# Optimization experiments

Measured on AMD Instinct MI355X. Metric: run time of the kernel, lower is better.

The kernel has to match this reference:

```python
import jax, jax.numpy as jnp
import numpy as np

B, TQ, M, D, H, F, L = 4, 512, 512, 1024, 16, 4096, 6
S = D // H
R = TQ + M  # relative-attention length = memory + query
CUTOFFS = [20000, 40000, 200000]
PROJ_FACTOR = 4
LN_EPS = 1e-6
NEG_INF = -1e9


def setup_inputs() -> dict:
    key = jax.random.key(0)
    ks = iter(jax.random.split(key, 64))

    def w(shape, scale=0.02):
        return jax.random.normal(next(ks), shape, jnp.float32) * scale

    inp = {}
    inp['token_ids'] = jax.random.randint(next(ks), (B, TQ), 0, CUTOFFS[-1])
    inp['memories'] = w((L, B, M, D))
    starts = [0] + CUTOFFS
    pf = 1
    for i in range(len(CUTOFFS)):
        psize = max(1, D // pf)
        inp['emb_table%d' % i] = w((starts[i + 1] - starts[i], psize))
        inp['emb_proj%d' % i] = w((psize, D))
        pf *= PROJ_FACTOR
    inp['wq'] = w((L, D, H, S)); inp['wk'] = w((L, D, H, S))
    inp['wv'] = w((L, D, H, S)); inp['wr'] = w((L, D, H, S))
    inp['wo'] = w((L, H, S, D))
    inp['content_bias'] = w((L, H, S)); inp['position_bias'] = w((L, H, S))
    inp['ln1_scale'] = jnp.ones((L, D)); inp['ln1_bias'] = jnp.zeros((L, D))
    inp['ln2_scale'] = jnp.ones((L, D)); inp['ln2_bias'] = jnp.zeros((L, D))
    inp['ffn_w1'] = w((L, D, F)); inp['ffn_b1'] = jnp.zeros((L, F))
    inp['ffn_w2'] = w((L, F, D)); inp['ffn_b2'] = jnp.zeros((L, D))
    return inp


def layernorm(x, scale, bias):
    mu = jnp.mean(x, axis=-1, keepdims=True)
    var = jnp.var(x, axis=-1, keepdims=True)
    return (x - mu) * jax.lax.rsqrt(var + LN_EPS) * scale + bias


def rel_shift(x):
    # x: [B, H, Q, R] -> shifted so position j aligns with relative distance
    b, h, q, r = x.shape
    x = jnp.pad(x, ((0, 0), (0, 0), (0, 0), (1, 0)))
    x = x.reshape(b, h, r + 1, q)[:, :, 1:, :]
    return x.reshape(b, h, q, r)


def positional_encoding(r_len, d):
    pos = jnp.arange(r_len - 1, -1, -1, dtype=jnp.float32)  # r_len-1 ... 0
    inv_freq = 1.0 / (10000.0 ** (jnp.arange(0, d, 2, dtype=jnp.float32) / d))
    sinusoid = pos[:, None] * inv_freq[None, :]
    return jnp.concatenate([jnp.sin(sinusoid), jnp.cos(sinusoid)], axis=-1)


def adaptive_embed(ids, tables, projs):
    # jit-friendly version of AdaptiveEmbedding.compute_embeddings:
    # gather per-cluster, project up to D, combine via masks.
    d = projs[0].shape[-1]
    y = jnp.zeros(ids.shape + (d,), jnp.float32)
    starts = [0] + CUTOFFS
    for tab, proj, lo, hi in zip(tables, projs, starts[:-1], starts[1:]):
        mask = (ids >= lo) & (ids < hi)
        idx = jnp.clip(ids - lo, 0, tab.shape[0] - 1)
        emb = jnp.einsum('btp,pd->btd', tab[idx], proj)
        y = y + jnp.where(mask[..., None], emb, 0.0)
    return y * (d ** 0.5)


def transformer_xl(token_ids, memories, emb_tables, emb_projs, wq, wk, wv, wr,
                   wo, content_bias, position_bias, ln1_scale, ln1_bias,
                   ln2_scale, ln2_bias, ffn_w1, ffn_b1, ffn_w2, ffn_b2):
    x = adaptive_embed(token_ids, emb_tables, emb_projs)  # [B, TQ, D]
    pe = positional_encoding(R, D)                        # [R, D]
    q_idx = jnp.arange(TQ)[:, None]
    r_idx = jnp.arange(R)[None, :]
    future = r_idx > q_idx + M                            # [TQ, R], True=masked
    scale = 1.0 / np.sqrt(S).astype(np.float32)
    for l in range(L):
        q = jnp.einsum('btd,dhs->bths', x, wq[l])
        kv_in = jnp.concatenate([memories[l], x], axis=1)  # [B, R, D]
        k = jnp.einsum('brd,dhs->brhs', kv_in, wk[l])
        v = jnp.einsum('brd,dhs->brhs', kv_in, wv[l])
        r = jnp.einsum('rd,dhs->rhs', pe, wr[l])
        ac = jnp.einsum('bqhs,brhs->bhqr', q + content_bias[l], k)
        bd = rel_shift(jnp.einsum('bqhs,rhs->bhqr', q + position_bias[l], r))
        scores = (ac + bd) * scale
        scores = jnp.where(future[None, None], NEG_INF, scores)
        attn = jax.nn.softmax(scores, axis=-1)
        ctx = jnp.einsum('bhqr,brhs->bqhs', attn, v)
        out = jnp.einsum('bqhs,hsd->bqd', ctx, wo[l])
        x = layernorm(x + out, ln1_scale[l], ln1_bias[l])
        h = jax.nn.relu(jnp.einsum('btd,df->btf', x, ffn_w1[l]) + ffn_b1[l])
        h = jnp.einsum('btf,fd->btd', h, ffn_w2[l]) + ffn_b2[l]
        x = layernorm(x + h, ln2_scale[l], ln2_bias[l])
    return x


def reference(token_ids, memories, emb_table0, emb_proj0, emb_table1,
              emb_proj1, emb_table2, emb_proj2, wq, wk, wv, wr, wo,
              content_bias, position_bias, ln1_scale, ln1_bias, ln2_scale,
              ln2_bias, ffn_w1, ffn_b1, ffn_w2, ffn_b2):
    return transformer_xl(
        token_ids, memories,
        [emb_table0, emb_table1, emb_table2],
        [emb_proj0, emb_proj1, emb_proj2],
        wq, wk, wv, wr, wo, content_bias, position_bias,
        ln1_scale, ln1_bias, ln2_scale, ln2_bias,
        ffn_w1, ffn_b1, ffn_w2, ffn_b2)
```

## Files before the change

kernel.cpp:

```cpp
#include <hip/hip_runtime.h>


#define Bc 4
#define TQc 512
#define Mc 512
#define Dc 1024
#define Hc 16
#define Sc 64
#define Fc 4096
#define Lc 6
#define Rc 1024
#define KCAT 1344
#define DDc ((size_t)Dc * Dc)
#define NEG_INF_F (-1e9f)

typedef unsigned short ushortT;
typedef __attribute__((ext_vector_type(8))) short bfrag;
typedef __attribute__((ext_vector_type(4))) float facc;

__device__ inline ushortT f2bf(float f) {
    unsigned int u = __builtin_bit_cast(unsigned int, f);
    u = (u + 0x7FFFu + ((u >> 16) & 1u)) >> 16;
    return (ushortT)u;
}

#define CP16(gp, lp)                                                        \
    __builtin_amdgcn_global_load_lds(                                       \
        (const __attribute__((address_space(1))) unsigned int*)(gp),        \
        (__attribute__((address_space(3))) unsigned int*)(lp), 16, 0, 0)

__device__ inline bfrag lds_frag(const ushortT* lds, int row, int cg) {
    int c = cg ^ (row & 7);
    return *reinterpret_cast<const bfrag*>(
        reinterpret_cast<const char*>(lds) + row * 128 + c * 16);
}

template<int BM, int BN, int OUTM, bool BIAS, bool RELU, bool DUALQ,
         bool KVSRC = false, bool KVOUT = false>
__global__ __launch_bounds__(256) void mgemm(
    const ushortT* __restrict__ A, const ushortT* __restrict__ A2,
    const ushortT* __restrict__ Bt,
    const float* __restrict__ bias, const float* __restrict__ bias2,
    float* __restrict__ Cf, ushortT* __restrict__ Cb, ushortT* __restrict__ Cb2,
    int K, int lda, int ldb, int ldc,
    long long sA1, long long sB1, long long sC1, float oscale) {
    constexpr int WTM = BM / 2, WTN = BN / 2;
    constexpr int FM = WTM / 16, FN = WTN / 16;
    __shared__ ushortT sA[2][BM * 64];
    __shared__ ushortT sB[2][BN * 64];
    int tid = threadIdx.x;
    int wave = tid >> 6, lane = tid & 63;
    int r16 = lane & 15, kgrp = lane >> 4;
    int wr = wave >> 1, wc = wave & 1;
    int z = blockIdx.z;
    A  += (long long)z * sA1;
    Bt += (long long)z * sB1;
    long long coff = (long long)z * sC1;
    if (OUTM != 1) Cf += coff;
    if (OUTM != 0 || DUALQ) Cb += coff;

    int row0 = blockIdx.y * BM, col0 = blockIdx.x * BN;
    facc acc[FM][FN] = {};

    auto STAGE = [&](int buf, int k0) {
        #pragma unroll
        for (int it = 0; it < BM / 32; ++it) {
            int s = it * 256 + tid;
            int row = s >> 3, c = s & 7;
            int cs = c ^ (row & 7);
            const char* g;
            if constexpr (KVSRC) {
                int arow = row0 + row;
                int bq = arow >> 10;
                int r = arow & 1023;
                if (r < Mc)
                    g = (const char*)(A + ((size_t)bq * Mc + r) * lda + k0) + cs * 16;
                else
                    g = (const char*)(A2 + ((size_t)bq * TQc + (r - Mc)) * lda + k0) + cs * 16;
            } else {
                g = (const char*)(A + (size_t)(row0 + row) * lda + k0) + cs * 16;
            }
            CP16(g, (char*)sA[buf] + s * 16);
        }
        #pragma unroll
        for (int it = 0; it < BN / 32; ++it) {
            int s = it * 256 + tid;
            int row = s >> 3, c = s & 7;
            int cs = c ^ (row & 7);
            CP16((const char*)(Bt + (size_t)(col0 + row) * ldb + k0) + cs * 16,
                 (char*)sB[buf] + s * 16);
        }
    };

    STAGE(0, 0);
    __syncthreads();
    int nk = K >> 6;
    for (int t = 0; t < nk; ++t) {
        int cur = t & 1;
        if (t + 1 < nk) STAGE(cur ^ 1, (t + 1) << 6);
        #pragma unroll
        for (int ks = 0; ks < 2; ++ks) {
            bfrag af[FM], bf[FN];
            #pragma unroll
            for (int mi = 0; mi < FM; ++mi)
                af[mi] = lds_frag(sA[cur], wr * WTM + mi * 16 + r16, ks * 4 + kgrp);
            #pragma unroll
            for (int ni = 0; ni < FN; ++ni)
                bf[ni] = lds_frag(sB[cur], wc * WTN + ni * 16 + r16, ks * 4 + kgrp);
            #pragma unroll
            for (int mi = 0; mi < FM; ++mi)
                #pragma unroll
                for (int ni = 0; ni < FN; ++ni)
                    acc[mi][ni] = __builtin_amdgcn_mfma_f32_16x16x32_bf16(
                        af[mi], bf[ni], acc[mi][ni], 0, 0, 0);
        }
        __syncthreads();
    }

    if constexpr (KVOUT) {
        if (col0 >= 1024) {
            ushortT* sT = (ushortT*)sA;
            int b = row0 >> 10, r0l = row0 & 1023;
            int h0 = (col0 - 1024) >> 6;
            #pragma unroll
            for (int p = 0; p < 2; ++p) {
                __syncthreads();
                if (wc == p) {
                    #pragma unroll
                    for (int mi = 0; mi < FM; ++mi)
                        #pragma unroll
                        for (int ni = 0; ni < FN; ++ni) {
                            int srow = ni * 16 + r16;
                            int cbase = wr * 64 + mi * 16 + kgrp * 4;
                            short4 s4;
                            s4.x = (short)f2bf(acc[mi][ni][0]);
                            s4.y = (short)f2bf(acc[mi][ni][1]);
                            s4.z = (short)f2bf(acc[mi][ni][2]);
                            s4.w = (short)f2bf(acc[mi][ni][3]);
                            *(short4*)(sT + srow * 132 + cbase) = s4;
                        }
                }
                __syncthreads();
                int h = h0 + p;
                #pragma unroll
                for (int it = 0; it < 4; ++it) {
                    int srow = it * 16 + (tid >> 4);
                    int rch = (tid & 15) * 8;
                    short4 lo = *(short4*)(sT + srow * 132 + rch);
                    short4 hi = *(short4*)(sT + srow * 132 + rch + 4);
                    ushortT* dst = Cb2 + ((size_t)((b * 16 + h) * 64 + srow)) * Rc
                                   + r0l + rch;
                    *(short4*)dst = lo;
                    *(short4*)(dst + 4) = hi;
                }
            }
            return;
        }
    }

    #pragma unroll
    for (int mi = 0; mi < FM; ++mi) {
        #pragma unroll
        for (int ni = 0; ni < FN; ++ni) {
            int gcol = col0 + wc * WTN + ni * 16 + r16;
            float bv = 0.0f, bv2 = 0.0f;
            if (BIAS || DUALQ) bv = bias[gcol];
            if (DUALQ) bv2 = bias2[gcol];
            #pragma unroll
            for (int j = 0; j < 4; ++j) {
                int grow = row0 + wr * WTM + mi * 16 + kgrp * 4 + j;
                float v = acc[mi][ni][j];
                if constexpr (DUALQ) {
                    Cb [(size_t)grow * ldc + gcol] = f2bf((v + bv) * oscale);
                    Cb2[(size_t)grow * ldc + gcol] = f2bf((v + bv2) * oscale);
                } else if constexpr (OUTM == 2) {
                    v *= oscale;
                    Cf[(size_t)grow * ldc + gcol] = v;
                    Cb[(size_t)grow * ldc + gcol] = f2bf(v);
                } else {
                    if (BIAS) v += bv;
                    if (RELU) v = fmaxf(v, 0.0f);
                    if constexpr (OUTM == 0)
                        Cf[(size_t)grow * ldc + gcol] = v;
                    else
                        Cb[(size_t)grow * ldc + gcol] = f2bf(v);
                }
            }
        }
    }
}

__global__ __launch_bounds__(256) void fused_attn(
    const ushortT* __restrict__ qc, const ushortT* __restrict__ qp,
    const ushortT* __restrict__ kb, const ushortT* __restrict__ vT,
    const ushortT* __restrict__ rp, ushortT* __restrict__ ctx) {
    int qt = blockIdx.x;
    int bh = blockIdx.y;
    int b = bh >> 4, h = bh & 15;
    int q0 = qt * 64;
    __shared__ ushortT sQc[64 * 64], sQp[64 * 64];
    __shared__ ushortT sK[64 * 64], sV[64 * 64], sP[64 * 64];
    __shared__ ushortT sR[128 * 64];
    __shared__ float sBD[64 * 65];
    int tid = threadIdx.x;
    int lane = tid & 63, wq = tid >> 6;
    int r16 = lane & 15, kgrp = lane >> 4;

    const ushortT* qcb = qc + (size_t)(b * TQc + q0) * Dc + h * 64;
    const ushortT* qpb = qp + (size_t)(b * TQc + q0) * Dc + h * 64;
    const ushortT* kbb = kb + (size_t)b * Rc * 1024 + h * 64;
    const ushortT* vTb = vT + (size_t)bh * 64 * Rc;
    const ushortT* rpb = rp + h * 64;
    int rrbase0 = 448 - q0;

    #pragma unroll
    for (int it = 0; it < 2; ++it) {
        int s = it * 256 + tid;
        int row = s >> 3, c = s & 7;
        int cs = c ^ (row & 7);
        CP16((const char*)(qcb + (size_t)row * Dc) + cs * 16, (char*)sQc + s * 16);
        CP16((const char*)(qpb + (size_t)row * Dc) + cs * 16, (char*)sQp + s * 16);
        CP16((const char*)(kbb + (size_t)row * 1024) + cs * 16, (char*)sK + s * 16);
        CP16((const char*)(vTb + (size_t)row * Rc) + cs * 16, (char*)sV + s * 16);
    }
    #pragma unroll
    for (int hR = 0; hR < 2; ++hR) {
        #pragma unroll
        for (int it = 0; it < 2; ++it) {
            int s = it * 256 + tid;
            int row = s >> 3, c = s & 7;
            int cs = c ^ (row & 7);
            int gr = rrbase0 + hR * 64 + row;
            gr = gr > 1023 ? 1023 : gr;
            CP16((const char*)(rpb + (size_t)gr * Dc) + cs * 16,
                 (char*)sR + (hR * 64 + row) * 128 + cs * 16);
        }
    }

    facc accO[4] = {};
    float m[4] = {-1e30f, -1e30f, -1e30f, -1e30f};
    float lsum[4] = {};

    int iters = qt + 9;
    for (int itj = 0; itj < iters; ++itj) {
        int j0 = itj * 64;
        __syncthreads();

        facc aac[4] = {};
        facc abd[8] = {};
        __builtin_amdgcn_s_setprio(1);
        #pragma unroll
        for (int ks = 0; ks < 2; ++ks) {
            bfrag aq = lds_frag(sQc, wq * 16 + r16, ks * 4 + kgrp);
            bfrag ap = lds_frag(sQp, wq * 16 + r16, ks * 4 + kgrp);
            #pragma unroll
            for (int n = 0; n < 4; ++n) {
                bfrag bk = lds_frag(sK, n * 16 + r16, ks * 4 + kgrp);
                aac[n] = __builtin_amdgcn_mfma_f32_16x16x32_bf16(aq, bk, aac[n], 0, 0, 0);
            }
            #pragma unroll
            for (int n = 0; n < 8; ++n) {
                int ph = (itj ^ (n >> 2)) & 1;
                bfrag br = lds_frag(sR, ph * 64 + (n & 3) * 16 + r16, ks * 4 + kgrp);
                abd[n] = __builtin_amdgcn_mfma_f32_16x16x32_bf16(ap, br, abd[n], 0, 0, 0);
            }
        }
        __builtin_amdgcn_s_setprio(0);
        #pragma unroll
        for (int n = 0; n < 8; ++n) {
            int rl = n * 16 + r16;
            #pragma unroll
            for (int jj = 0; jj < 4; ++jj) {
                int ql = wq * 16 + kgrp * 4 + jj;
                int jl = rl + ql - 63;
                if (jl >= 0 && jl < 64) sBD[ql * 65 + jl] = abd[n][jj];
            }
        }

        float P[4][4];
        #pragma unroll
        for (int jj = 0; jj < 4; ++jj) {
            int ql = wq * 16 + kgrp * 4 + jj;
            int qg = q0 + ql;
            float sv[4];
            float mx = -3e38f;
            #pragma unroll
            for (int n = 0; n < 4; ++n) {
                int jl = n * 16 + r16;
                int jg = j0 + jl;
                float s = aac[n][jj] + sBD[ql * 65 + jl];
                if (jg > qg + Mc) s = NEG_INF_F;
                sv[n] = s;
                mx = fmaxf(mx, s);
            }
            mx = fmaxf(mx, __shfl_xor(mx, 1));
            mx = fmaxf(mx, __shfl_xor(mx, 2));
            mx = fmaxf(mx, __shfl_xor(mx, 4));
            mx = fmaxf(mx, __shfl_xor(mx, 8));
            float mnew = fmaxf(m[jj], mx);
            float corr = __expf(m[jj] - mnew);
            m[jj] = mnew;
            float rs = 0.0f;
            #pragma unroll
            for (int n = 0; n < 4; ++n) {
                float p = __expf(sv[n] - mnew);
                P[n][jj] = p;
                rs += p;
            }
            rs += __shfl_xor(rs, 1);
            rs += __shfl_xor(rs, 2);
            rs += __shfl_xor(rs, 4);
            rs += __shfl_xor(rs, 8);
            lsum[jj] = lsum[jj] * corr + rs;
            #pragma unroll
            for (int n = 0; n < 4; ++n) accO[n][jj] *= corr;
        }
        #pragma unroll
        for (int jj = 0; jj < 4; ++jj) {
            int row = wq * 16 + kgrp * 4 + jj;
            #pragma unroll
            for (int n = 0; n < 4; ++n) {
                int col = n * 16 + r16;
                int boff = row * 128 + (((col >> 3) ^ (row & 7)) * 16) + (col & 7) * 2;
                *(ushortT*)((char*)sP + boff) = f2bf(P[n][jj]);
            }
        }
        __builtin_amdgcn_s_setprio(1);
        #pragma unroll
        for (int ks = 0; ks < 2; ++ks) {
            bfrag pa = lds_frag(sP, wq * 16 + r16, ks * 4 + kgrp);
            #pragma unroll
            for (int n = 0; n < 4; ++n) {
                bfrag bv = lds_frag(sV, n * 16 + r16, ks * 4 + kgrp);
                accO[n] = __builtin_amdgcn_mfma_f32_16x16x32_bf16(pa, bv, accO[n], 0, 0, 0);
            }
        }
        __builtin_amdgcn_s_setprio(0);
        __syncthreads();

        if (itj + 1 < iters) {
            int jn = j0 + 64;
            #pragma unroll
            for (int it2 = 0; it2 < 2; ++it2) {
                int s = it2 * 256 + tid;
                int row = s >> 3, c = s & 7;
                int cs = c ^ (row & 7);
                CP16((const char*)(kbb + (size_t)(jn + row) * 1024) + cs * 16,
                     (char*)sK + s * 16);
                CP16((const char*)(vTb + (size_t)row * Rc + jn) + cs * 16,
                     (char*)sV + s * 16);
            }
            int ph = itj & 1;
            int grb = jn - q0 + 512;
            #pragma unroll
            for (int it2 = 0; it2 < 2; ++it2) {
                int s = it2 * 256 + tid;
                int row = s >> 3, c = s & 7;
                int cs = c ^ (row & 7);
                int gr = grb + row;
                gr = gr > 1023 ? 1023 : gr;
                CP16((const char*)(rpb + (size_t)gr * Dc) + cs * 16,
                     (char*)sR + (ph * 64 + row) * 128 + cs * 16);
            }
        }
    }
    #pragma unroll
    for (int jj = 0; jj < 4; ++jj) {
        int qg = q0 + wq * 16 + kgrp * 4 + jj;
        float inv = 1.0f / lsum[jj];
        #pragma unroll
        for (int n = 0; n < 4; ++n) {
            int col = n * 16 + r16;
            ctx[(size_t)(b * TQc + qg) * Dc + h * 64 + col] = f2bf(accO[n][jj] * inv);
        }
    }
}

__global__ __launch_bounds__(256) void tr_f32_bf16(
    const float* __restrict__ in, ushortT* __restrict__ out, int R0, int C0,
    int ldout, int coff, long long inZ, long long outZ) {
    in += (long long)blockIdx.z * inZ;
    out += (long long)blockIdx.z * outZ;
    __shared__ float t[32][33];
    int tx = threadIdx.x & 31, ty = threadIdx.x >> 5;
    int c0 = blockIdx.x * 32, r0 = blockIdx.y * 32;
    #pragma unroll
    for (int i = 0; i < 4; ++i)
        t[ty + i * 8][tx] = in[(size_t)(r0 + ty + i * 8) * C0 + c0 + tx];
    __syncthreads();
    #pragma unroll
    for (int i = 0; i < 4; ++i)
        out[(size_t)(c0 + ty + i * 8) * ldout + coff + r0 + tx] = f2bf(t[tx][ty + i * 8]);
}

__global__ __launch_bounds__(256) void tr_dxd5(
    const float* __restrict__ wr, const float* __restrict__ wq,
    const float* __restrict__ wk, const float* __restrict__ wv,
    const float* __restrict__ wo,
    ushortT* __restrict__ wrT, ushortT* __restrict__ wqT,
    ushortT* __restrict__ wkvT, ushortT* __restrict__ woT) {
    int sel = blockIdx.z / Lc, l = blockIdx.z % Lc;
    const float* in; ushortT* out;
    if (sel == 0)      { in = wr + l * DDc; out = wrT + l * DDc; }
    else if (sel == 1) { in = wq + l * DDc; out = wqT + l * DDc; }
    else if (sel == 2) { in = wk + l * DDc; out = wkvT + l * 2 * DDc; }
    else if (sel == 3) { in = wv + l * DDc; out = wkvT + l * 2 * DDc + DDc; }
    else               { in = wo + l * DDc; out = woT + l * DDc; }
    __shared__ float t[32][33];
    int tx = threadIdx.x & 31, ty = threadIdx.x >> 5;
    int c0 = blockIdx.x * 32, r0 = blockIdx.y * 32;
    #pragma unroll
    for (int i = 0; i < 4; ++i)
        t[ty + i * 8][tx] = in[(size_t)(r0 + ty + i * 8) * Dc + c0 + tx];
    __syncthreads();
    #pragma unroll
    for (int i = 0; i < 4; ++i)
        out[(size_t)(c0 + ty + i * 8) * Dc + r0 + tx] = f2bf(t[tx][ty + i * 8]);
}

__global__ __launch_bounds__(256) void pos_enc_kernel(ushortT* __restrict__ pe) {
    int idx = blockIdx.x * 256 + threadIdx.x;
    int r = idx >> 10;
    int d = idx & 1023;
    float pos = (float)(Rc - 1 - r);
    int i = (d < 512) ? d : (d - 512);
    float inv_freq = 1.0f / powf(10000.0f, (2.0f * (float)i) / 1024.0f);
    float arg = pos * inv_freq;
    pe[idx] = f2bf((d < 512) ? sinf(arg) : cosf(arg));
}

__global__ __launch_bounds__(256) void gather_embed(
    const int* __restrict__ ids,
    const float* __restrict__ t0, const float* __restrict__ t1,
    const float* __restrict__ t2, ushortT* __restrict__ gcat) {
    int token = blockIdx.x;
    int id = ids[token];
    ushortT* row = gcat + (size_t)token * KCAT;
    short4 z4 = {0, 0, 0, 0};
    for (int t = threadIdx.x; t < KCAT / 4; t += 256)
        reinterpret_cast<short4*>(row)[t] = z4;
    __syncthreads();
    const float* tab; int psize, lo, o;
    if (id < 20000)      { tab = t0; psize = 1024; lo = 0;     o = 0; }
    else if (id < 40000) { tab = t1; psize = 256;  lo = 20000; o = 1024; }
    else                 { tab = t2; psize = 64;   lo = 40000; o = 1280; }
    const float* src = tab + (size_t)(id - lo) * psize;
    for (int p4 = threadIdx.x; p4 < psize / 4; p4 += 256) {
        float4 v = reinterpret_cast<const float4*>(src)[p4];
        short4 s4;
        s4.x = (short)f2bf(v.x); s4.y = (short)f2bf(v.y);
        s4.z = (short)f2bf(v.z); s4.w = (short)f2bf(v.w);
        reinterpret_cast<short4*>(row + o)[p4] = s4;
    }
}

__global__ __launch_bounds__(256) void cast_f32_bf16(
    const float* __restrict__ in, ushortT* __restrict__ o) {
    size_t i8 = ((size_t)blockIdx.x * 256 + threadIdx.x) * 8;
    const float4* m4 = (const float4*)(in + i8);
    float4 a = m4[0], c = m4[1];
    int4 p;
    p.x = (int)f2bf(a.x) | ((int)f2bf(a.y) << 16);
    p.y = (int)f2bf(a.z) | ((int)f2bf(a.w) << 16);
    p.z = (int)f2bf(c.x) | ((int)f2bf(c.y) << 16);
    p.w = (int)f2bf(c.z) | ((int)f2bf(c.w) << 16);
    *(int4*)(o + i8) = p;
}

template<int NP, bool CBIAS>
__global__ __launch_bounds__(256) void add_ln_kernel(
    const float* __restrict__ xin, const float* __restrict__ r0,
    const float* __restrict__ r1, const float* __restrict__ r2,
    const float* __restrict__ r3, const float* __restrict__ cbias,
    const float* __restrict__ scale, const float* __restrict__ bias,
    float* __restrict__ dst, ushortT* __restrict__ dstb) {
    int row = blockIdx.x * 4 + (threadIdx.x >> 6);
    int lane = threadIdx.x & 63;
    const float4* xr = (const float4*)(xin + (size_t)row * Dc);
    const float4* p0 = (const float4*)(r0 + (size_t)row * Dc);
    const float4* p1 = nullptr; const float4* p2 = nullptr; const float4* p3 = nullptr;
    if constexpr (NP > 1) {
        p1 = (const float4*)(r1 + (size_t)row * Dc);
        p2 = (const float4*)(r2 + (size_t)row * Dc);
        p3 = (const float4*)(r3 + (size_t)row * Dc);
    }
    const float4* cb4 = CBIAS ? (const float4*)cbias : nullptr;
    float4 v[4];
    float s = 0.0f, s2 = 0.0f;
    #pragma unroll
    for (int rep = 0; rep < 4; ++rep) {
        int idx = rep * 64 + lane;
        float4 a = xr[idx];
        float4 b = p0[idx];
        a.x += b.x; a.y += b.y; a.z += b.z; a.w += b.w;
        if constexpr (NP > 1) {
            float4 c1 = p1[idx], c2 = p2[idx], c3 = p3[idx];
            a.x += c1.x + c2.x + c3.x; a.y += c1.y + c2.y + c3.y;
            a.z += c1.z + c2.z + c3.z; a.w += c1.w + c2.w + c3.w;
        }
        if constexpr (CBIAS) {
            float4 cbv = cb4[idx];
            a.x += cbv.x; a.y += cbv.y; a.z += cbv.z; a.w += cbv.w;
        }
        v[rep] = a;
        s += a.x + a.y + a.z + a.w;
        s2 += a.x * a.x + a.y * a.y + a.z * a.z + a.w * a.w;
    }
    #pragma unroll
    for (int o = 1; o < 64; o <<= 1) {
        s += __shfl_xor(s, o);
        s2 += __shfl_xor(s2, o);
    }
    float mean = s * (1.0f / Dc);
    float var = s2 * (1.0f / Dc) - mean * mean;
    float rstd = rsqrtf(var + 1e-6f);
    float4* d4 = (float4*)(dst + (size_t)row * Dc);
    short4* db4 = (short4*)(dstb + (size_t)row * Dc);
    const float4* sc4 = (const float4*)scale;
    const float4* bi4 = (const float4*)bias;
    #pragma unroll
    for (int rep = 0; rep < 4; ++rep) {
        int idx = rep * 64 + lane;
        float4 scv = sc4[idx], biv = bi4[idx];
        float4 a = v[rep];
        float4 o;
        o.x = (a.x - mean) * rstd * scv.x + biv.x;
        o.y = (a.y - mean) * rstd * scv.y + biv.y;
        o.z = (a.z - mean) * rstd * scv.z + biv.z;
        o.w = (a.w - mean) * rstd * scv.w + biv.w;
        d4[idx] = o;
        short4 ob;
        ob.x = (short)f2bf(o.x); ob.y = (short)f2bf(o.y);
        ob.z = (short)f2bf(o.z); ob.w = (short)f2bf(o.w);
        db4[idx] = ob;
    }
}

extern "C" void kernel_launch(void* const* d_in, const int* in_sizes, int n_in,
                              void* d_out, int out_size, void* d_ws, size_t ws_size,
                              hipStream_t stream) {
    const int*   token_ids = (const int*)d_in[0];
    const float* memories  = (const float*)d_in[1];
    const float* tab0 = (const float*)d_in[2];
    const float* prj0 = (const float*)d_in[3];
    const float* tab1 = (const float*)d_in[4];
    const float* prj1 = (const float*)d_in[5];
    const float* tab2 = (const float*)d_in[6];
    const float* prj2 = (const float*)d_in[7];
    const float* wq = (const float*)d_in[8];
    const float* wk = (const float*)d_in[9];
    const float* wv = (const float*)d_in[10];
    const float* wr = (const float*)d_in[11];
    const float* wo = (const float*)d_in[12];
    const float* cb = (const float*)d_in[13];
    const float* pb = (const float*)d_in[14];
    const float* ln1s = (const float*)d_in[15];
    const float* ln1b = (const float*)d_in[16];
    const float* ln2s = (const float*)d_in[17];
    const float* ln2b = (const float*)d_in[18];
    const float* w1 = (const float*)d_in[19];
    const float* b1 = (const float*)d_in[20];
    const float* w2 = (const float*)d_in[21];
    const float* b2 = (const float*)d_in[22];
    float* out = (float*)d_out;

    char* wsb = (char*)d_ws;
    size_t off = 0;
    auto alloc = [&](size_t bytes) {
        char* p = wsb + off;
        off += (bytes + 255) & ~(size_t)255;
        return p;
    };
    const size_t DD = DDc;
    const size_t TD = (size_t)Bc * TQc * Dc;
    const size_t DF = (size_t)Dc * Fc;
    ushortT* pe_b  = (ushortT*)alloc((size_t)Rc * Dc * 2);
    ushortT* wrT   = (ushortT*)alloc((size_t)Lc * DD * 2);
    ushortT* rpA   = (ushortT*)alloc((size_t)Lc * Rc * Dc * 2);
    ushortT* wqT   = (ushortT*)alloc((size_t)Lc * DD * 2);
    ushortT* wkvT  = (ushortT*)alloc((size_t)Lc * 2 * DD * 2);
    ushortT* woT   = (ushortT*)alloc((size_t)Lc * DD * 2);
    ushortT* w1T   = (ushortT*)alloc((size_t)Lc * DF * 2);
    ushortT* w2T   = (ushortT*)alloc((size_t)Lc * DF * 2);
    ushortT* memb  = (ushortT*)alloc((size_t)Lc * Bc * Mc * Dc * 2);
    ushortT* gcat  = (ushortT*)alloc((size_t)Bc * TQc * KCAT * 2);
    ushortT* WcatT = (ushortT*)alloc((size_t)Dc * KCAT * 2);
    float*   x     = (float*)alloc(TD * 4);
    ushortT* xb    = (ushortT*)alloc(TD * 2);
    ushortT* qc    = (ushortT*)alloc(TD * 2);
    ushortT* qp    = (ushortT*)alloc(TD * 2);
    ushortT* kbuf  = (ushortT*)alloc((size_t)Bc * Rc * 1024 * 2);
    ushortT* vT    = (ushortT*)alloc((size_t)Bc * Rc * Dc * 2);
    ushortT* ctxb  = (ushortT*)alloc(TD * 2);
    float*   obp   = (float*)alloc(4 * TD * 4);
    ushortT* hb    = (ushortT*)alloc((size_t)Bc * TQc * Fc * 2);

    pos_enc_kernel<<<(Rc * Dc) / 256, 256, 0, stream>>>(pe_b);
    gather_embed<<<Bc * TQc, 256, 0, stream>>>(token_ids, tab0, tab1, tab2, gcat);
    tr_f32_bf16<<<dim3(32, 32), 256, 0, stream>>>(prj0, WcatT, 1024, 1024, KCAT, 0, 0, 0);
    tr_f32_bf16<<<dim3(32, 8), 256, 0, stream>>>(prj1, WcatT, 256, 1024, KCAT, 1024, 0, 0);
    tr_f32_bf16<<<dim3(32, 2), 256, 0, stream>>>(prj2, WcatT, 64, 1024, KCAT, 1280, 0, 0);
    mgemm<64, 64, 2, false, false, false><<<dim3(16, 32), 256, 0, stream>>>(
        gcat, nullptr, WcatT, nullptr, nullptr, x, xb, nullptr,
        KCAT, KCAT, KCAT, Dc, 0, 0, 0, 32.0f);

    tr_dxd5<<<dim3(32, 32, 5 * Lc), 256, 0, stream>>>(
        wr, wq, wk, wv, wo, wrT, wqT, wkvT, woT);
    tr_f32_bf16<<<dim3(128, 32, Lc), 256, 0, stream>>>(w1, w1T, Dc, Fc, Dc, 0, DF, DF);
    tr_f32_bf16<<<dim3(32, 128, Lc), 256, 0, stream>>>(w2, w2T, Fc, Dc, Fc, 0, DF, DF);
    cast_f32_bf16<<<(Lc * Bc * Mc * Dc) / (256 * 8), 256, 0, stream>>>(memories, memb);
    mgemm<64, 64, 1, false, false, false><<<dim3(16, 16, Lc), 256, 0, stream>>>(
        pe_b, nullptr, wrT, nullptr, nullptr, nullptr, rpA, nullptr,
        Dc, Dc, Dc, Dc, 0, (long long)DD, (long long)Rc * Dc, 1.0f);

    for (int l = 0; l < Lc; ++l) {
        const ushortT* membl = memb + (size_t)l * Bc * Mc * Dc;
        mgemm<64, 64, 1, false, false, true><<<dim3(16, 32), 256, 0, stream>>>(
            xb, nullptr, wqT + (size_t)l * DD, cb + (size_t)l * Dc, pb + (size_t)l * Dc,
            nullptr, qc, qp, Dc, Dc, Dc, Dc, 0, 0, 0, 0.125f);
        mgemm<128, 128, 1, false, false, false, true, true>
            <<<dim3(16, 32), 256, 0, stream>>>(
            membl, xb, wkvT + (size_t)l * 2 * DD, nullptr, nullptr,
            nullptr, kbuf, vT, Dc, Dc, Dc, 1024, 0, 0, 0, 1.0f);

        fused_attn<<<dim3(8, 64), 256, 0, stream>>>(
            qc, qp, kbuf, vT, rpA + (size_t)l * Rc * Dc, ctxb);

        mgemm<64, 64, 0, false, false, false><<<dim3(16, 32), 256, 0, stream>>>(
            ctxb, nullptr, woT + (size_t)l * DD, nullptr, nullptr, obp, nullptr, nullptr,
            Dc, Dc, Dc, Dc, 0, 0, 0, 1.0f);
        add_ln_kernel<1, false><<<Bc * TQc / 4, 256, 0, stream>>>(
            x, obp, nullptr, nullptr, nullptr, nullptr,
            ln1s + (size_t)l * Dc, ln1b + (size_t)l * Dc, x, xb);
        mgemm<128, 128, 1, true, true, false><<<dim3(32, 16), 256, 0, stream>>>(
            xb, nullptr, w1T + (size_t)l * DF, b1 + (size_t)l * Fc, nullptr,
            nullptr, hb, nullptr, Dc, Dc, Dc, Fc, 0, 0, 0, 1.0f);
        mgemm<128, 128, 0, false, false, false><<<dim3(8, 16, 4), 256, 0, stream>>>(
            hb, nullptr, w2T + (size_t)l * DF, nullptr, nullptr, obp, nullptr, nullptr,
            1024, Fc, Fc, Dc, 1024, 1024, (long long)TD, 1.0f);
        add_ln_kernel<4, true><<<Bc * TQc / 4, 256, 0, stream>>>(
            x, obp, obp + TD, obp + 2 * TD, obp + 3 * TD, b2 + (size_t)l * Dc,
            ln2s + (size_t)l * Dc, ln2b + (size_t)l * Dc,
            (l == Lc - 1) ? out : x, xb);
    }
}
```

Before: 1.318 ms.

## Retune GEMM tiles, halve FFN2 split-K, remap attention blocks, vectorize transposes

Several unrelated changes at once. The 1024-wide GEMMs move from 64x64 to 128x64 tiles, and the FFN2 split-K drops from 4 to 2 partitions, so add_ln reads two partial sums instead of four. The attention grid is remapped so that light and heavy query tiles are interleaved across workgroups, and the causal mask is applied only on the last key iteration. The transpose kernels now write packed short4 stores instead of scalar ones. The aim is fewer launched blocks, less partial-sum traffic, better load balance and cheaper stores, at the cost of lower occupancy per GEMM and less parallelism in FFN2.

```diff
diff --git a/kernel.cpp b/kernel.cpp
--- a/kernel.cpp
+++ b/kernel.cpp
@@ -194,8 +194,11 @@
     const ushortT* __restrict__ qc, const ushortT* __restrict__ qp,
     const ushortT* __restrict__ kb, const ushortT* __restrict__ vT,
     const ushortT* __restrict__ rp, ushortT* __restrict__ ctx) {
-    int qt = blockIdx.x;
-    int bh = blockIdx.y;
+    int n_id = (int)(blockIdx.y << 3) | (int)blockIdx.x;
+    int b0 = n_id & 1, b7 = (n_id >> 7) & 1, b8 = (n_id >> 8) & 1;
+    int u = (b7 << 1) | b0;
+    int qt = (b0 ^ b8) ? (7 - u) : u;
+    int bh = (n_id >> 1) & 63;
     int b = bh >> 4, h = bh & 15;
     int q0 = qt * 64;
     __shared__ ushortT sQc[64 * 64], sQp[64 * 64];
@@ -277,22 +280,26 @@
             }
         }
 
+        bool lastit = (itj == iters - 1);
         float P[4][4];
         #pragma unroll
         for (int jj = 0; jj < 4; ++jj) {
             int ql = wq * 16 + kgrp * 4 + jj;
-            int qg = q0 + ql;
             float sv[4];
-            float mx = -3e38f;
             #pragma unroll
             for (int n = 0; n < 4; ++n) {
                 int jl = n * 16 + r16;
-                int jg = j0 + jl;
-                float s = aac[n][jj] + sBD[ql * 65 + jl];
-                if (jg > qg + Mc) s = NEG_INF_F;
-                sv[n] = s;
-                mx = fmaxf(mx, s);
-            }
+                sv[n] = aac[n][jj] + sBD[ql * 65 + jl];
+            }
+            if (lastit) {
+                int qg = q0 + ql;
+                #pragma unroll
+                for (int n = 0; n < 4; ++n) {
+                    int jg = j0 + n * 16 + r16;
+                    if (jg > qg + Mc) sv[n] = NEG_INF_F;
+                }
+            }
+            float mx = fmaxf(fmaxf(sv[0], sv[1]), fmaxf(sv[2], sv[3]));
             mx = fmaxf(mx, __shfl_xor(mx, 1));
             mx = fmaxf(mx, __shfl_xor(mx, 2));
             mx = fmaxf(mx, __shfl_xor(mx, 4));
@@ -388,9 +395,13 @@
     for (int i = 0; i < 4; ++i)
         t[ty + i * 8][tx] = in[(size_t)(r0 + ty + i * 8) * C0 + c0 + tx];
     __syncthreads();
-    #pragma unroll
-    for (int i = 0; i < 4; ++i)
-        out[(size_t)(c0 + ty + i * 8) * ldout + coff + r0 + tx] = f2bf(t[tx][ty + i * 8]);
+    int c = threadIdx.x >> 3, rq = (threadIdx.x & 7) << 2;
+    short4 s4;
+    s4.x = (short)f2bf(t[rq + 0][c]);
+    s4.y = (short)f2bf(t[rq + 1][c]);
+    s4.z = (short)f2bf(t[rq + 2][c]);
+    s4.w = (short)f2bf(t[rq + 3][c]);
+    *(short4*)(out + (size_t)(c0 + c) * ldout + coff + r0 + rq) = s4;
 }
 
 __global__ __launch_bounds__(256) void tr_dxd5(
@@ -413,9 +424,13 @@
     for (int i = 0; i < 4; ++i)
         t[ty + i * 8][tx] = in[(size_t)(r0 + ty + i * 8) * Dc + c0 + tx];
     __syncthreads();
-    #pragma unroll
-    for (int i = 0; i < 4; ++i)
-        out[(size_t)(c0 + ty + i * 8) * Dc + r0 + tx] = f2bf(t[tx][ty + i * 8]);
+    int c = threadIdx.x >> 3, rq = (threadIdx.x & 7) << 2;
+    short4 s4;
+    s4.x = (short)f2bf(t[rq + 0][c]);
+    s4.y = (short)f2bf(t[rq + 1][c]);
+    s4.z = (short)f2bf(t[rq + 2][c]);
+    s4.w = (short)f2bf(t[rq + 3][c]);
+    *(short4*)(out + (size_t)(c0 + c) * Dc + r0 + rq) = s4;
 }
 
 __global__ __launch_bounds__(256) void pos_enc_kernel(ushortT* __restrict__ pe) {
@@ -479,11 +494,9 @@
     const float4* xr = (const float4*)(xin + (size_t)row * Dc);
     const float4* p0 = (const float4*)(r0 + (size_t)row * Dc);
     const float4* p1 = nullptr; const float4* p2 = nullptr; const float4* p3 = nullptr;
-    if constexpr (NP > 1) {
-        p1 = (const float4*)(r1 + (size_t)row * Dc);
-        p2 = (const float4*)(r2 + (size_t)row * Dc);
-        p3 = (const float4*)(r3 + (size_t)row * Dc);
-    }
+    if constexpr (NP > 1) p1 = (const float4*)(r1 + (size_t)row * Dc);
+    if constexpr (NP > 2) p2 = (const float4*)(r2 + (size_t)row * Dc);
+    if constexpr (NP > 3) p3 = (const float4*)(r3 + (size_t)row * Dc);
     const float4* cb4 = CBIAS ? (const float4*)cbias : nullptr;
     float4 v[4];
     float s = 0.0f, s2 = 0.0f;
@@ -494,9 +507,16 @@
         float4 b = p0[idx];
         a.x += b.x; a.y += b.y; a.z += b.z; a.w += b.w;
         if constexpr (NP > 1) {
-            float4 c1 = p1[idx], c2 = p2[idx], c3 = p3[idx];
-            a.x += c1.x + c2.x + c3.x; a.y += c1.y + c2.y + c3.y;
-            a.z += c1.z + c2.z + c3.z; a.w += c1.w + c2.w + c3.w;
+            float4 c1 = p1[idx];
+            a.x += c1.x; a.y += c1.y; a.z += c1.z; a.w += c1.w;
+        }
+        if constexpr (NP > 2) {
+            float4 c2 = p2[idx];
+            a.x += c2.x; a.y += c2.y; a.z += c2.z; a.w += c2.w;
+        }
+        if constexpr (NP > 3) {
+            float4 c3 = p3[idx];
+            a.x += c3.x; a.y += c3.y; a.z += c3.z; a.w += c3.w;
         }
         if constexpr (CBIAS) {
             float4 cbv = cb4[idx];
@@ -600,7 +620,7 @@
     tr_f32_bf16<<<dim3(32, 32), 256, 0, stream>>>(prj0, WcatT, 1024, 1024, KCAT, 0, 0, 0);
     tr_f32_bf16<<<dim3(32, 8), 256, 0, stream>>>(prj1, WcatT, 256, 1024, KCAT, 1024, 0, 0);
     tr_f32_bf16<<<dim3(32, 2), 256, 0, stream>>>(prj2, WcatT, 64, 1024, KCAT, 1280, 0, 0);
-    mgemm<64, 64, 2, false, false, false><<<dim3(16, 32), 256, 0, stream>>>(
+    mgemm<128, 64, 2, false, false, false><<<dim3(16, 16), 256, 0, stream>>>(
         gcat, nullptr, WcatT, nullptr, nullptr, x, xb, nullptr,
         KCAT, KCAT, KCAT, Dc, 0, 0, 0, 32.0f);
 
@@ -609,13 +629,13 @@
     tr_f32_bf16<<<dim3(128, 32, Lc), 256, 0, stream>>>(w1, w1T, Dc, Fc, Dc, 0, DF, DF);
     tr_f32_bf16<<<dim3(32, 128, Lc), 256, 0, stream>>>(w2, w2T, Fc, Dc, Fc, 0, DF, DF);
     cast_f32_bf16<<<(Lc * Bc * Mc * Dc) / (256 * 8), 256, 0, stream>>>(memories, memb);
-    mgemm<64, 64, 1, false, false, false><<<dim3(16, 16, Lc), 256, 0, stream>>>(
+    mgemm<128, 64, 1, false, false, false><<<dim3(16, 8, Lc), 256, 0, stream>>>(
         pe_b, nullptr, wrT, nullptr, nullptr, nullptr, rpA, nullptr,
         Dc, Dc, Dc, Dc, 0, (long long)DD, (long long)Rc * Dc, 1.0f);
 
     for (int l = 0; l < Lc; ++l) {
         const ushortT* membl = memb + (size_t)l * Bc * Mc * Dc;
-        mgemm<64, 64, 1, false, false, true><<<dim3(16, 32), 256, 0, stream>>>(
+        mgemm<128, 64, 1, false, false, true><<<dim3(16, 16), 256, 0, stream>>>(
             xb, nullptr, wqT + (size_t)l * DD, cb + (size_t)l * Dc, pb + (size_t)l * Dc,
             nullptr, qc, qp, Dc, Dc, Dc, Dc, 0, 0, 0, 0.125f);
         mgemm<128, 128, 1, false, false, false, true, true>
@@ -626,7 +646,7 @@
         fused_attn<<<dim3(8, 64), 256, 0, stream>>>(
             qc, qp, kbuf, vT, rpA + (size_t)l * Rc * Dc, ctxb);
 
-        mgemm<64, 64, 0, false, false, false><<<dim3(16, 32), 256, 0, stream>>>(
+        mgemm<128, 64, 0, false, false, false><<<dim3(16, 16), 256, 0, stream>>>(
             ctxb, nullptr, woT + (size_t)l * DD, nullptr, nullptr, obp, nullptr, nullptr,
             Dc, Dc, Dc, Dc, 0, 0, 0, 1.0f);
         add_ln_kernel<1, false><<<Bc * TQc / 4, 256, 0, stream>>>(
@@ -635,11 +655,11 @@
         mgemm<128, 128, 1, true, true, false><<<dim3(32, 16), 256, 0, stream>>>(
             xb, nullptr, w1T + (size_t)l * DF, b1 + (size_t)l * Fc, nullptr,
             nullptr, hb, nullptr, Dc, Dc, Dc, Fc, 0, 0, 0, 1.0f);
-        mgemm<128, 128, 0, false, false, false><<<dim3(8, 16, 4), 256, 0, stream>>>(
+        mgemm<128, 128, 0, false, false, false><<<dim3(8, 16, 2), 256, 0, stream>>>(
             hb, nullptr, w2T + (size_t)l * DF, nullptr, nullptr, obp, nullptr, nullptr,
-            1024, Fc, Fc, Dc, 1024, 1024, (long long)TD, 1.0f);
-        add_ln_kernel<4, true><<<Bc * TQc / 4, 256, 0, stream>>>(
-            x, obp, obp + TD, obp + 2 * TD, obp + 3 * TD, b2 + (size_t)l * Dc,
+            2048, Fc, Fc, Dc, 2048, 2048, (long long)TD, 1.0f);
+        add_ln_kernel<2, true><<<Bc * TQc / 4, 256, 0, stream>>>(
+            x, obp, obp + TD, nullptr, nullptr, b2 + (size_t)l * Dc,
             ln2s + (size_t)l * Dc, ln2b + (size_t)l * Dc,
             (l == Lc - 1) ? out : x, xb);
     }
```

Result: slower. 1.394 ms (+5.8%).
